# Performance work log

Hardware: AMD Instinct MI355X
Metric: run time of the kernel (lower is better)

The kernel has to match this reference:

```python
import jax, jax.numpy as jnp
import numpy as np

L, E, H, T, B = 8, 1024, 16, 2048, 1
DH = E // H
LN_EPS = 1e-5
MASKED_BIAS = -10000.0


def setup_inputs() -> dict:
    key = jax.random.key(0)
    ks = jax.random.split(key, 6)
    std = 0.02
    return {
        "x": jax.random.normal(ks[0], (B, T, E), jnp.float32),
        "ln1_w": jnp.ones((L, E), jnp.float32),
        "ln1_b": jnp.zeros((L, E), jnp.float32),
        "attn_w": std * jax.random.normal(ks[1], (L, E, 3 * E), jnp.float32),
        "attn_b": jnp.zeros((L, 3 * E), jnp.float32),
        "proj_w": std * jax.random.normal(ks[2], (L, E, E), jnp.float32),
        "proj_b": jnp.zeros((L, E), jnp.float32),
        "ln2_w": jnp.ones((L, E), jnp.float32),
        "ln2_b": jnp.zeros((L, E), jnp.float32),
        "fc_w": std * jax.random.normal(ks[3], (L, E, 4 * E), jnp.float32),
        "fc_b": jnp.zeros((L, 4 * E), jnp.float32),
        "fc2_w": std * jax.random.normal(ks[4], (L, 4 * E, E), jnp.float32),
        "fc2_b": jnp.zeros((L, E), jnp.float32),
    }


def _layernorm(h, w, b):
    mu = jnp.mean(h, axis=-1, keepdims=True)
    var = jnp.mean(jnp.square(h - mu), axis=-1, keepdims=True)
    return (h - mu) * jax.lax.rsqrt(var + LN_EPS) * w + b


def _gpt2_stack(x, ln1_w, ln1_b, attn_w, attn_b, proj_w, proj_b,
                ln2_w, ln2_b, fc_w, fc_b, fc2_w, fc2_b):
    b, t, e = x.shape
    causal = jnp.tril(jnp.ones((t, t), dtype=bool))  # [T,T] tril mask buffer
    scale = 1.0 / jnp.sqrt(jnp.float32(DH))          # scale=True -> 1/sqrt(head_dim)

    def block(h, p):
        l1w, l1b, aw, ab, pw, pb, l2w, l2b, fw, fb, f2w, f2b = p
        # masked self-attention
        y = _layernorm(h, l1w, l1b)
        qkv = y @ aw + ab                              # [B,T,3E]
        q, k, v = jnp.split(qkv, 3, axis=-1)
        sh = lambda z: z.reshape(b, t, H, DH).transpose(0, 2, 1, 3)  # [B,H,T,DH]
        q, k, v = sh(q), sh(k), sh(v)
        w = jnp.einsum("bhqd,bhkd->bhqk", q, k) * scale
        w = jnp.where(causal, w, jnp.float32(MASKED_BIAS))
        w = jax.nn.softmax(w, axis=-1)
        a = jnp.einsum("bhqk,bhkd->bhqd", w, v)
        a = a.transpose(0, 2, 1, 3).reshape(b, t, e)   # merge heads
        a = a @ pw + pb
        h = h + a
        # MLP (gelu_new = tanh-approx gelu)
        y = _layernorm(h, l2w, l2b)
        m = jax.nn.gelu(y @ fw + fb, approximate=True) @ f2w + f2b
        return h + m, None

    out, _ = jax.lax.scan(
        block, x,
        (ln1_w, ln1_b, attn_w, attn_b, proj_w, proj_b,
         ln2_w, ln2_b, fc_w, fc_b, fc2_w, fc2_b))
    return out


def reference(x, ln1_w, ln1_b, attn_w, attn_b, proj_w, proj_b,
              ln2_w, ln2_b, fc_w, fc_b, fc2_w, fc2_b):
    return _gpt2_stack(x, ln1_w, ln1_b, attn_w, attn_b, proj_w, proj_b,
                       ln2_w, ln2_b, fc_w, fc_b, fc2_w, fc2_b)
```

## Files before the change

kernel.cpp:

```cpp
#include <hip/hip_runtime.h>
#include <cstdint>

typedef short s16x8 __attribute__((ext_vector_type(8)));
typedef __bf16 b16x8 __attribute__((ext_vector_type(8)));
typedef float f32x4 __attribute__((ext_vector_type(4)));

#define TSEQ 2048
#define EDIM 1024

__device__ __forceinline__ short f2bf(float x) {
  unsigned u = __float_as_uint(x);
  unsigned r = (u + 0x7FFFu + ((u >> 16) & 1u)) >> 16;
  return (short)r;
}

__device__ __forceinline__ f32x4 mfma16(s16x8 a, s16x8 b, f32x4 c) {
  return __builtin_amdgcn_mfma_f32_16x16x32_bf16(
      __builtin_bit_cast(b16x8, a), __builtin_bit_cast(b16x8, b), c, 0, 0, 0);
}

__device__ __forceinline__ void gl_lds16(void* lds, const void* g) {
  __builtin_amdgcn_global_load_lds(
      (const __attribute__((address_space(1))) void*)g,
      (__attribute__((address_space(3))) void*)lds, 16, 0, 0);
}

__global__ __launch_bounds__(256) void cvtT(
    const float* __restrict__ W, short* __restrict__ WT, int K, int N) {
  int t = blockIdx.x;
  const int tn = N >> 5;
  const int bn = (t % tn) << 5, bk = (t / tn) << 5;
  __shared__ float tile[32][33];
  const int tx = threadIdx.x & 31, ty = threadIdx.x >> 5;
#pragma unroll
  for (int i = 0; i < 4; ++i)
    tile[ty + i * 8][tx] = W[(size_t)(bk + ty + i * 8) * N + bn + tx];
  __syncthreads();
#pragma unroll
  for (int i = 0; i < 4; ++i)
    WT[(size_t)(bn + ty + i * 8) * K + bk + tx] = f2bf(tile[tx][ty + i * 8]);
}

__global__ __launch_bounds__(256) void ln_kernel(
    const float* __restrict__ h, const float* __restrict__ w,
    const float* __restrict__ b, short* __restrict__ y) {
  const int row = blockIdx.x, tid = threadIdx.x;
  const float4 v = ((const float4*)(h + (size_t)row * EDIM))[tid];
  float s = v.x + v.y + v.z + v.w;
  float s2 = v.x * v.x + v.y * v.y + v.z * v.z + v.w * v.w;
#pragma unroll
  for (int off = 1; off < 64; off <<= 1) {
    s += __shfl_xor(s, off, 64);
    s2 += __shfl_xor(s2, off, 64);
  }
  __shared__ float red[8];
  const int wave = tid >> 6, lane = tid & 63;
  if (lane == 0) { red[wave] = s; red[4 + wave] = s2; }
  __syncthreads();
  s = red[0] + red[1] + red[2] + red[3];
  s2 = red[4] + red[5] + red[6] + red[7];
  const float mu = s * (1.f / EDIM);
  const float var = s2 * (1.f / EDIM) - mu * mu;
  const float rstd = rsqrtf(var + 1e-5f);
  const float4 wv = ((const float4*)w)[tid];
  const float4 bv = ((const float4*)b)[tid];
  short4 o = make_short4(f2bf((v.x - mu) * rstd * wv.x + bv.x),
                         f2bf((v.y - mu) * rstd * wv.y + bv.y),
                         f2bf((v.z - mu) * rstd * wv.z + bv.z),
                         f2bf((v.w - mu) * rstd * wv.w + bv.w));
  ((short4*)(y + (size_t)row * EDIM))[tid] = o;
}

template <int EPI, int BM>
__global__ __launch_bounds__(256, 2) void gemm_bt(
    const short* __restrict__ A, const short* __restrict__ BT,
    const float* __restrict__ bias, short* __restrict__ out_bf,
    short* __restrict__ vt, float* __restrict__ out_f,
    const float* __restrict__ resid, int M, int N, int K) {
  constexpr int WM = BM / 2;
  constexpr int NMI = WM / 16;
  __shared__ __align__(16) short As[BM * 32];
  __shared__ __align__(16) short Bs[128 * 32];
  const int tid = threadIdx.x;
  const int wave = tid >> 6, lane = tid & 63;
  const int quad = lane >> 4, l16 = lane & 15;
  const int wr = (wave >> 1) * WM, wc = (wave & 1) * 64;
  const int m0 = blockIdx.y * BM, n0 = blockIdx.x * 128;

  const int srow = tid >> 2, scol = (tid & 3) * 8;
  const short* Ag = A + (size_t)(m0 + srow) * K + scol;
  const short* Bg = BT + (size_t)(n0 + srow) * K + scol;
  short* As0 = &As[wave * 512];
  short* Bs0 = &Bs[wave * 512];
  short* Bs1 = &Bs[2048 + wave * 512];

  f32x4 acc[NMI][4] = {};
  for (int k0 = 0; k0 < K; k0 += 32) {
    gl_lds16(As0, Ag + k0);
    if (BM == 128) gl_lds16(&As[2048 + wave * 512], Ag + (size_t)64 * K + k0);
    gl_lds16(Bs0, Bg + k0);
    gl_lds16(Bs1, Bg + (size_t)64 * K + k0);
    __syncthreads();
    s16x8 af[NMI], bfr[4];
#pragma unroll
    for (int i = 0; i < NMI; ++i)
      af[i] = *(const s16x8*)&As[(wr + i * 16 + l16) * 32 + quad * 8];
#pragma unroll
    for (int i = 0; i < 4; ++i)
      bfr[i] = *(const s16x8*)&Bs[(wc + i * 16 + l16) * 32 + quad * 8];
#pragma unroll
    for (int mi = 0; mi < NMI; ++mi)
#pragma unroll
      for (int ni = 0; ni < 4; ++ni)
        acc[mi][ni] = mfma16(af[mi], bfr[ni], acc[mi][ni]);
    __syncthreads();
  }

#pragma unroll
  for (int mi = 0; mi < NMI; ++mi) {
#pragma unroll
    for (int ni = 0; ni < 4; ++ni) {
      const int col = n0 + wc + ni * 16 + l16;
      const float bv = bias[col];
#pragma unroll
      for (int r = 0; r < 4; ++r) {
        const int row = m0 + wr + mi * 16 + quad * 4 + r;
        float v = acc[mi][ni][r] + bv;
        if (EPI == 1) {
          const size_t idx = (size_t)row * N + col;
          out_f[idx] = v + resid[idx];
        } else if (EPI == 2) {
          const float u = 0.7978845608028654f * (v + 0.044715f * v * v * v);
          out_bf[(size_t)row * N + col] = f2bf(0.5f * v * (1.f + tanhf(u)));
        } else {
          if (col < 2048)
            out_bf[(size_t)row * 2048 + col] = f2bf(v);
          else
            vt[(size_t)(col - 2048) * TSEQ + row] = f2bf(v);
        }
      }
    }
  }
}

__global__ __launch_bounds__(256) void attn_fused(
    const short* __restrict__ qk,
    const short* __restrict__ vt,
    short* __restrict__ aout) {
  const int head = blockIdx.y;
  const int sidx = (blockIdx.x + 4 * (head & 7)) & 31;
  const int qg = (head < 8) ? sidx : 31 - sidx;
  const int qbase = qg << 6;
  const int qt_end = qg >> 1;

  const int tid = threadIdx.x;
  const int wave = tid >> 6, lane = tid & 63;
  const int quad = lane >> 4, l16 = lane & 15;
  const int qrow = qbase + wave * 16;

  __shared__ __align__(16) short Ks[128 * 64];
  __shared__ __align__(16) short Vs[64 * 128];
  __shared__ __align__(16) short ps[4][16 * 136];
  short* psw = ps[wave];

  s16x8 qf[2];
#pragma unroll
  for (int ks = 0; ks < 2; ++ks)
    qf[ks] = *(const s16x8*)&qk[(size_t)(qrow + l16) * 2048 +
                                head * 64 + ks * 32 + quad * 8];

  const int krow_off = tid >> 3;
  const int kchk = ((tid & 7) ^ (krow_off & 7)) * 8;
  const int vrow_off = tid >> 4;
  const int vchk = ((tid & 15) ^ vrow_off) * 8;

  const float scale = 0.125f;
  float mrow[4], lrow[4];
  f32x4 oacc[4] = {};
#pragma unroll
  for (int r = 0; r < 4; ++r) { mrow[r] = -1e30f; lrow[r] = 0.f; }

  for (int kt = 0; kt <= qt_end; ++kt) {
    const int k0 = kt << 7;
#pragma unroll
    for (int c = 0; c < 4; ++c) {
      gl_lds16(&Ks[c * 2048 + wave * 512],
               qk + (size_t)(k0 + c * 32 + krow_off) * 2048 + 1024 + head * 64 + kchk);
      gl_lds16(&Vs[c * 2048 + wave * 512],
               vt + (size_t)(head * 64 + c * 16 + vrow_off) * TSEQ + k0 + vchk);
    }
    __syncthreads();

    f32x4 s[8] = {};
    __builtin_amdgcn_s_setprio(1);
#pragma unroll
    for (int ni = 0; ni < 8; ++ni) {
      const int kr = ni * 16 + l16;
      const int sw = kr & 7;
      s16x8 kf0 = *(const s16x8*)((const char*)Ks + kr * 128 + ((quad ^ sw) << 4));
      s16x8 kf1 = *(const s16x8*)((const char*)Ks + kr * 128 + ((quad ^ 4 ^ sw) << 4));
      s[ni] = mfma16(qf[0], kf0, s[ni]);
      s[ni] = mfma16(qf[1], kf1, s[ni]);
    }
    __builtin_amdgcn_s_setprio(0);

    const bool diag = (kt == qt_end);
    float rmax[4] = {-1e30f, -1e30f, -1e30f, -1e30f};
#pragma unroll
    for (int ni = 0; ni < 8; ++ni)
#pragma unroll
      for (int r = 0; r < 4; ++r) {
        float v = s[ni][r] * scale;
        if (diag) {
          const int qa = qrow + quad * 4 + r;
          const int ka = k0 + ni * 16 + l16;
          if (ka > qa) v = -1e30f;
        }
        s[ni][r] = v;
        rmax[r] = fmaxf(rmax[r], v);
      }
#pragma unroll
    for (int off = 1; off < 16; off <<= 1)
#pragma unroll
      for (int r = 0; r < 4; ++r)
        rmax[r] = fmaxf(rmax[r], __shfl_xor(rmax[r], off, 64));
    float al[4];
#pragma unroll
    for (int r = 0; r < 4; ++r) {
      const float mnew = fmaxf(mrow[r], rmax[r]);
      al[r] = __expf(mrow[r] - mnew);
      mrow[r] = mnew;
      lrow[r] *= al[r];
    }
#pragma unroll
    for (int ni = 0; ni < 4; ++ni)
#pragma unroll
      for (int r = 0; r < 4; ++r) oacc[ni][r] *= al[r];
    float psum[4] = {};
#pragma unroll
    for (int ni = 0; ni < 8; ++ni)
#pragma unroll
      for (int r = 0; r < 4; ++r) {
        const float p = __expf(s[ni][r] - mrow[r]);
        psum[r] += p;
        psw[(quad * 4 + r) * 136 + ni * 16 + l16] = f2bf(p);
      }
#pragma unroll
    for (int off = 1; off < 16; off <<= 1)
#pragma unroll
      for (int r = 0; r < 4; ++r) psum[r] += __shfl_xor(psum[r], off, 64);
#pragma unroll
    for (int r = 0; r < 4; ++r) lrow[r] += psum[r];

    __builtin_amdgcn_s_setprio(1);
#pragma unroll
    for (int ks = 0; ks < 4; ++ks) {
      s16x8 pa = *(const s16x8*)&psw[l16 * 136 + ks * 32 + quad * 8];
#pragma unroll
      for (int ni = 0; ni < 4; ++ni) {
        const int vr = ni * 16 + l16;
        s16x8 vf = *(const s16x8*)((const char*)Vs + vr * 256 +
                                   ((((ks << 2) | quad) ^ (vr & 15)) << 4));
        oacc[ni] = mfma16(pa, vf, oacc[ni]);
      }
    }
    __builtin_amdgcn_s_setprio(0);
    __syncthreads();
  }

#pragma unroll
  for (int ni = 0; ni < 4; ++ni)
#pragma unroll
    for (int r = 0; r < 4; ++r) {
      const int qa = qrow + quad * 4 + r;
      aout[(size_t)qa * EDIM + head * 64 + ni * 16 + l16] =
          f2bf(oacc[ni][r] / lrow[r]);
    }
}

extern "C" void kernel_launch(void* const* d_in, const int* in_sizes, int n_in,
                              void* d_out, int out_size, void* d_ws, size_t ws_size,
                              hipStream_t stream) {
  const float* x     = (const float*)d_in[0];
  const float* ln1w  = (const float*)d_in[1];
  const float* ln1b  = (const float*)d_in[2];
  const float* attw  = (const float*)d_in[3];
  const float* attb  = (const float*)d_in[4];
  const float* projw = (const float*)d_in[5];
  const float* projb = (const float*)d_in[6];
  const float* ln2w  = (const float*)d_in[7];
  const float* ln2b  = (const float*)d_in[8];
  const float* fcw   = (const float*)d_in[9];
  const float* fcb   = (const float*)d_in[10];
  const float* fc2w  = (const float*)d_in[11];
  const float* fc2b  = (const float*)d_in[12];

  char* ws = (char*)d_ws;
  float* h   = (float*)(ws);
  short* y   = (short*)(ws + (8u << 20));
  short* att = (short*)(ws + (8u << 20));
  short* qkb = (short*)(ws + (12u << 20));
  short* vt  = (short*)(ws + (20u << 20));
  short* mid = (short*)(ws + (12u << 20));
  short* wT  = (short*)(ws + (28u << 20));

  hipMemcpyAsync(h, x, (size_t)TSEQ * EDIM * 4, hipMemcpyDeviceToDevice, stream);

  for (int l = 0; l < 8; ++l) {
    ln_kernel<<<TSEQ, 256, 0, stream>>>(h, ln1w + l * 1024, ln1b + l * 1024, y);
    cvtT<<<(3072 / 32) * (1024 / 32), 256, 0, stream>>>(
        attw + (size_t)l * 1024 * 3072, wT, 1024, 3072);
    gemm_bt<0, 128><<<dim3(24, 16), 256, 0, stream>>>(
        y, wT, attb + l * 3072, qkb, vt, nullptr, nullptr, 2048, 3072, 1024);
    attn_fused<<<dim3(32, 16), 256, 0, stream>>>(qkb, vt, att);
    cvtT<<<(1024 / 32) * (1024 / 32), 256, 0, stream>>>(
        projw + (size_t)l * 1024 * 1024, wT, 1024, 1024);
    gemm_bt<1, 64><<<dim3(8, 32), 256, 0, stream>>>(
        att, wT, projb + l * 1024, nullptr, nullptr, h, h, 2048, 1024, 1024);
    ln_kernel<<<TSEQ, 256, 0, stream>>>(h, ln2w + l * 1024, ln2b + l * 1024, y);
    cvtT<<<(4096 / 32) * (1024 / 32), 256, 0, stream>>>(
        fcw + (size_t)l * 1024 * 4096, wT, 1024, 4096);
    gemm_bt<2, 128><<<dim3(32, 16), 256, 0, stream>>>(
        y, wT, fcb + l * 4096, mid, nullptr, nullptr, nullptr, 2048, 4096, 1024);
    cvtT<<<(1024 / 32) * (4096 / 32), 256, 0, stream>>>(
        fc2w + (size_t)l * 4096 * 1024, wT, 4096, 1024);
    gemm_bt<1, 64><<<dim3(8, 32), 256, 0, stream>>>(
        mid, wT, fc2b + l * 1024, nullptr, nullptr, h, h, 2048, 1024, 4096);
  }

  hipMemcpyAsync(d_out, h, (size_t)TSEQ * EDIM * 4, hipMemcpyDeviceToDevice, stream);
}
```

Measured before the change: 2.181 ms.

## Double-buffer GEMM with swizzled 64-wide K tiles, split-K atomics, fast tanh

The bf16 GEMM now loads 64-wide K tiles into double-buffered LDS with an XOR swizzle, so the next tile's global-to-LDS loads overlap MFMA work on the current one and LDS bank conflicts drop. The residual GEMMs (proj and fc2) split K across two blocks in z and accumulate into the residual buffer with float atomicAdd; only the z=0 block adds the bias. This gives those small grids more blocks but makes the fp32 summation order nondeterministic. The GELU epilogue replaces tanhf with an exp-based formula, and the doubled LDS footprint may lower occupancy.

Measured after the change: 1.827 ms. -16.2%, faster.

```diff
diff --git a/kernel.cpp b/kernel.cpp
--- a/kernel.cpp
+++ b/kernel.cpp
@@ -76,44 +76,75 @@
     const short* __restrict__ A, const short* __restrict__ BT,
     const float* __restrict__ bias, short* __restrict__ out_bf,
     short* __restrict__ vt, float* __restrict__ out_f,
-    const float* __restrict__ resid, int M, int N, int K) {
+    int M, int N, int K) {
   constexpr int WM = BM / 2;
   constexpr int NMI = WM / 16;
-  __shared__ __align__(16) short As[BM * 32];
-  __shared__ __align__(16) short Bs[128 * 32];
+  constexpr int ASZ = BM * 64;
+  constexpr int BSZ = 128 * 64;
+  __shared__ __align__(16) short As[2 * ASZ];
+  __shared__ __align__(16) short Bs[2 * BSZ];
   const int tid = threadIdx.x;
   const int wave = tid >> 6, lane = tid & 63;
   const int quad = lane >> 4, l16 = lane & 15;
   const int wr = (wave >> 1) * WM, wc = (wave & 1) * 64;
   const int m0 = blockIdx.y * BM, n0 = blockIdx.x * 128;
-
-  const int srow = tid >> 2, scol = (tid & 3) * 8;
-  const short* Ag = A + (size_t)(m0 + srow) * K + scol;
-  const short* Bg = BT + (size_t)(n0 + srow) * K + scol;
-  short* As0 = &As[wave * 512];
-  short* Bs0 = &Bs[wave * 512];
-  short* Bs1 = &Bs[2048 + wave * 512];
+  const int ksplit = K / gridDim.z;
+  const int kbase = blockIdx.z * ksplit;
+
+  const int r8 = lane >> 3, c8 = lane & 7;
+  const int csw = (c8 ^ r8) << 3;
+  const short* Ag = A + (size_t)(m0 + wave * (BM / 4) + r8) * K + kbase + csw;
+  const short* Bg = BT + (size_t)(n0 + wave * 32 + r8) * K + kbase + csw;
 
   f32x4 acc[NMI][4] = {};
-  for (int k0 = 0; k0 < K; k0 += 32) {
-    gl_lds16(As0, Ag + k0);
-    if (BM == 128) gl_lds16(&As[2048 + wave * 512], Ag + (size_t)64 * K + k0);
-    gl_lds16(Bs0, Bg + k0);
-    gl_lds16(Bs1, Bg + (size_t)64 * K + k0);
+  const int NT = ksplit >> 6;
+
+#pragma unroll
+  for (int c = 0; c < BM / 32; ++c)
+    gl_lds16(&As[(wave * (BM / 32) + c) * 512], Ag + (size_t)(8 * c) * K);
+#pragma unroll
+  for (int c = 0; c < 4; ++c)
+    gl_lds16(&Bs[(wave * 4 + c) * 512], Bg + (size_t)(8 * c) * K);
+  __syncthreads();
+
+  int cur = 0;
+  for (int t = 0; t < NT; ++t) {
+    if (t + 1 < NT) {
+      const size_t ko = (size_t)(t + 1) << 6;
+#pragma unroll
+      for (int c = 0; c < BM / 32; ++c)
+        gl_lds16(&As[(cur ^ 1) * ASZ + (wave * (BM / 32) + c) * 512],
+                 Ag + (size_t)(8 * c) * K + ko);
+#pragma unroll
+      for (int c = 0; c < 4; ++c)
+        gl_lds16(&Bs[(cur ^ 1) * BSZ + (wave * 4 + c) * 512],
+                 Bg + (size_t)(8 * c) * K + ko);
+    }
+    const short* Ab = &As[cur * ASZ];
+    const short* Bb = &Bs[cur * BSZ];
+    const int rsw = l16 & 7;
+    s16x8 af[NMI][2], bfr[4][2];
+#pragma unroll
+    for (int i = 0; i < NMI; ++i)
+#pragma unroll
+      for (int ks = 0; ks < 2; ++ks)
+        af[i][ks] = *(const s16x8*)&Ab[(wr + i * 16 + l16) * 64 +
+                                       ((((ks << 2) | quad) ^ rsw) << 3)];
+#pragma unroll
+    for (int i = 0; i < 4; ++i)
+#pragma unroll
+      for (int ks = 0; ks < 2; ++ks)
+        bfr[i][ks] = *(const s16x8*)&Bb[(wc + i * 16 + l16) * 64 +
+                                        ((((ks << 2) | quad) ^ rsw) << 3)];
+#pragma unroll
+    for (int mi = 0; mi < NMI; ++mi)
+#pragma unroll
+      for (int ni = 0; ni < 4; ++ni)
+#pragma unroll
+        for (int ks = 0; ks < 2; ++ks)
+          acc[mi][ni] = mfma16(af[mi][ks], bfr[ni][ks], acc[mi][ni]);
     __syncthreads();
-    s16x8 af[NMI], bfr[4];
-#pragma unroll
-    for (int i = 0; i < NMI; ++i)
-      af[i] = *(const s16x8*)&As[(wr + i * 16 + l16) * 32 + quad * 8];
-#pragma unroll
-    for (int i = 0; i < 4; ++i)
-      bfr[i] = *(const s16x8*)&Bs[(wc + i * 16 + l16) * 32 + quad * 8];
-#pragma unroll
-    for (int mi = 0; mi < NMI; ++mi)
-#pragma unroll
-      for (int ni = 0; ni < 4; ++ni)
-        acc[mi][ni] = mfma16(af[mi], bfr[ni], acc[mi][ni]);
-    __syncthreads();
+    cur ^= 1;
   }
 
 #pragma unroll
@@ -121,17 +152,18 @@
 #pragma unroll
     for (int ni = 0; ni < 4; ++ni) {
       const int col = n0 + wc + ni * 16 + l16;
-      const float bv = bias[col];
+      const float bv = (EPI == 1 && blockIdx.z != 0) ? 0.f : bias[col];
 #pragma unroll
       for (int r = 0; r < 4; ++r) {
         const int row = m0 + wr + mi * 16 + quad * 4 + r;
         float v = acc[mi][ni][r] + bv;
         if (EPI == 1) {
-          const size_t idx = (size_t)row * N + col;
-          out_f[idx] = v + resid[idx];
+          atomicAdd(&out_f[(size_t)row * N + col], v);
         } else if (EPI == 2) {
           const float u = 0.7978845608028654f * (v + 0.044715f * v * v * v);
-          out_bf[(size_t)row * N + col] = f2bf(0.5f * v * (1.f + tanhf(u)));
+          const float e = __expf(2.f * u);
+          const float th = 1.f - 2.f / (e + 1.f);
+          out_bf[(size_t)row * N + col] = f2bf(0.5f * v * (1.f + th));
         } else {
           if (col < 2048)
             out_bf[(size_t)row * 2048 + col] = f2bf(v);
@@ -310,22 +342,22 @@
     ln_kernel<<<TSEQ, 256, 0, stream>>>(h, ln1w + l * 1024, ln1b + l * 1024, y);
     cvtT<<<(3072 / 32) * (1024 / 32), 256, 0, stream>>>(
         attw + (size_t)l * 1024 * 3072, wT, 1024, 3072);
-    gemm_bt<0, 128><<<dim3(24, 16), 256, 0, stream>>>(
-        y, wT, attb + l * 3072, qkb, vt, nullptr, nullptr, 2048, 3072, 1024);
+    gemm_bt<0, 128><<<dim3(24, 16, 1), 256, 0, stream>>>(
+        y, wT, attb + l * 3072, qkb, vt, nullptr, 2048, 3072, 1024);
     attn_fused<<<dim3(32, 16), 256, 0, stream>>>(qkb, vt, att);
     cvtT<<<(1024 / 32) * (1024 / 32), 256, 0, stream>>>(
         projw + (size_t)l * 1024 * 1024, wT, 1024, 1024);
-    gemm_bt<1, 64><<<dim3(8, 32), 256, 0, stream>>>(
-        att, wT, projb + l * 1024, nullptr, nullptr, h, h, 2048, 1024, 1024);
+    gemm_bt<1, 64><<<dim3(8, 32, 2), 256, 0, stream>>>(
+        att, wT, projb + l * 1024, nullptr, nullptr, h, 2048, 1024, 1024);
     ln_kernel<<<TSEQ, 256, 0, stream>>>(h, ln2w + l * 1024, ln2b + l * 1024, y);
     cvtT<<<(4096 / 32) * (1024 / 32), 256, 0, stream>>>(
         fcw + (size_t)l * 1024 * 4096, wT, 1024, 4096);
-    gemm_bt<2, 128><<<dim3(32, 16), 256, 0, stream>>>(
-        y, wT, fcb + l * 4096, mid, nullptr, nullptr, nullptr, 2048, 4096, 1024);
+    gemm_bt<2, 128><<<dim3(32, 16, 1), 256, 0, stream>>>(
+        y, wT, fcb + l * 4096, mid, nullptr, nullptr, 2048, 4096, 1024);
     cvtT<<<(1024 / 32) * (4096 / 32), 256, 0, stream>>>(
         fc2w + (size_t)l * 4096 * 1024, wT, 4096, 1024);
-    gemm_bt<1, 64><<<dim3(8, 32), 256, 0, stream>>>(
-        mid, wT, fc2b + l * 1024, nullptr, nullptr, h, h, 2048, 1024, 4096);
+    gemm_bt<1, 64><<<dim3(8, 32, 2), 256, 0, stream>>>(
+        mid, wT, fc2b + l * 1024, nullptr, nullptr, h, 2048, 1024, 4096);
   }
 
   hipMemcpyAsync(d_out, h, (size_t)TSEQ * EDIM * 4, hipMemcpyDeviceToDevice, stream);
```
